# Kernel tuning notes

Hardware: AMD Instinct MI355X
Metric: run time of the kernel (lower is better)

The kernel has to match this reference:

```python
import jax, jax.numpy as jnp
import numpy as np

B, C, H, W = 16, 384, 28, 28
F, E, FFN, NB, NH, WS = 384, 384, 1536, 12, 8, 7


def setup_inputs() -> dict:
    key = jax.random.key(0)
    ks = jax.random.split(key, 16)
    g = lambda k, s: (0.02 * jax.random.normal(k, s)).astype(jnp.float32)
    inp = {}
    inp['x'] = jax.random.normal(ks[0], (B, C, H, W), jnp.float32)
    # ViTInput params
    inp['embed_w'] = g(ks[1], (2, E))
    inp['embed_b'] = jnp.zeros((E,), jnp.float32)
    inp['in_w'] = g(ks[2], (E + C, F))
    inp['in_b'] = jnp.zeros((F,), jnp.float32)
    # per-block (stacked over NB) params
    inp['ln1_s'] = jnp.ones((NB, F), jnp.float32)
    inp['ln1_b'] = jnp.zeros((NB, F), jnp.float32)
    inp['qkv_w'] = g(ks[3], (NB, F, 3 * F))
    inp['qkv_b'] = jnp.zeros((NB, 3 * F), jnp.float32)
    inp['proj_w'] = g(ks[4], (NB, F, F))
    inp['proj_b'] = jnp.zeros((NB, F), jnp.float32)
    inp['ln2_s'] = jnp.ones((NB, F), jnp.float32)
    inp['ln2_b'] = jnp.zeros((NB, F), jnp.float32)
    inp['ffn_w1'] = g(ks[5], (NB, F, FFN))
    inp['ffn_b1'] = jnp.zeros((NB, FFN), jnp.float32)
    inp['ffn_w2'] = g(ks[6], (NB, FFN, F))
    inp['ffn_b2'] = jnp.zeros((NB, F), jnp.float32)
    # rezero alpha: torch inits to 0 (identity blocks); use 0.1 to exercise compute
    inp['re_alpha'] = 0.1 * jnp.ones((NB,), jnp.float32)
    # output projection
    inp['out_w'] = g(ks[7], (F, C))
    inp['out_b'] = jnp.zeros((C,), jnp.float32)
    return inp


def _ln(x, s, b, eps=1e-5):
    m = jnp.mean(x, axis=-1, keepdims=True)
    v = jnp.mean(jnp.square(x - m), axis=-1, keepdims=True)
    return (x - m) * jax.lax.rsqrt(v + eps) * s + b


def reference(x, embed_w, embed_b, in_w, in_b, ln1_s, ln1_b, qkv_w, qkv_b,
              proj_w, proj_b, ln2_s, ln2_b, ffn_w1, ffn_b1, ffn_w2, ffn_b2,
              re_alpha, out_w, out_b):
    Bn, Cn, Hn, Wn = x.shape
    L = Hn * Wn
    tokens = x.reshape(Bn, Cn, L).transpose(0, 2, 1)  # [B, L, C]
    # Fourier pos embed (torch.meshgrid(x, y) 'ij' then row-major flatten)
    xg = jnp.repeat(jnp.arange(Wn, dtype=jnp.float32), Hn)  # [L]
    yg = jnp.tile(jnp.arange(Hn, dtype=jnp.float32), Wn)    # [L]
    xn = 2.0 * xg / (Wn - 1) - 1.0
    yn = 2.0 * yg / (Hn - 1) - 1.0
    z = jnp.stack([xn, yn], axis=-1)                         # [L, 2]
    emb = jnp.sin(z @ embed_w + embed_b)                     # [L, E]
    emb = jnp.broadcast_to(emb[None], (Bn, L, emb.shape[-1]))
    h = jnp.concatenate([emb, tokens], axis=-1) @ in_w + in_b  # [B, L, F]

    Dh = F // NH
    nW = L // WS
    scale = 1.0 / jnp.sqrt(jnp.float32(Dh))

    def block(h, p):
        (l1s, l1b, qw, qb, pw, pb, l2s, l2b, w1, b1, w2, b2, alpha) = p
        y = _ln(h, l1s, l1b)
        qkv = y @ qw + qb                                   # [B, L, 3F]
        q, k, v = jnp.split(qkv, 3, axis=-1)
        hd = lambda t: t.reshape(Bn, nW, WS, NH, Dh)
        q, k, v = hd(q), hd(k), hd(v)
        att = jnp.einsum('bwqhd,bwkhd->bwhqk', q, k) * scale  # [B,nW,H,7,7]
        att = jax.nn.softmax(att, axis=-1)
        o = jnp.einsum('bwhqk,bwkhd->bwqhd', att, v).reshape(Bn, L, NH * Dh)
        o = o @ pw + pb
        h = h + alpha * o
        y2 = _ln(h, l2s, l2b)
        y2 = jax.nn.gelu(y2 @ w1 + b1, approximate=False) @ w2 + b2
        h = h + alpha * y2
        return h, None

    h, _ = jax.lax.scan(block, h, (ln1_s, ln1_b, qkv_w, qkv_b, proj_w, proj_b,
                                   ln2_s, ln2_b, ffn_w1, ffn_b1, ffn_w2, ffn_b2,
                                   re_alpha))
    out = h @ out_w + out_b                                  # [B, L, C]
    return out.transpose(0, 2, 1).reshape(Bn, Cn, Hn, Wn)
```

## Files before the change

kernel.cpp:

```cpp
#include <hip/hip_runtime.h>
#include <hip/hip_bf16.h>
#include <cstdint>
#include <cstddef>

#define BB 16
#define CC 384
#define LL 784
#define FF 384
#define EE 384
#define FFNx 1536
#define NB 12
#define NHEAD 8
#define MM (BB * LL)
#define MBY 98

typedef __attribute__((ext_vector_type(8))) short short8;
typedef __attribute__((ext_vector_type(4))) float floatx4;
typedef __attribute__((ext_vector_type(4))) unsigned int uintx4;

__device__ __forceinline__ float bf2f(uint16_t u) {
    union { unsigned int i; float f; } v; v.i = ((unsigned int)u) << 16; return v.f;
}
__device__ __forceinline__ uint16_t f2bf(float f) {
    union { float f; unsigned int i; } v; v.f = f;
    unsigned int r = v.i + 0x7fffu + ((v.i >> 16) & 1u);
    return (uint16_t)(r >> 16);
}
__device__ __forceinline__ float load_in(const void* p, size_t i, bool bf) {
    return bf ? bf2f(((const uint16_t*)p)[i]) : ((const float*)p)[i];
}
#define PROBE_BF(probe) (((const uint16_t*)(probe))[0] == 0x3F80u)

__device__ __forceinline__ void gload_lds16(const uint16_t* g, uint16_t* l) {
    __builtin_amdgcn_global_load_lds(
        (const __attribute__((address_space(1))) uint32_t*)g,
        (__attribute__((address_space(3))) uint32_t*)l,
        16, 0, 0);
}

__device__ __forceinline__ float gelu_f(float v) {
    float y = 0.7978845608028654f * (v + 0.044715f * v * v * v);
    y = fmaxf(y, -40.f);
    float e = __expf(-2.f * y);
    float th = (1.f - e) * __builtin_amdgcn_rcpf(1.f + e);
    return 0.5f * v * (1.f + th);
}

__global__ __launch_bounds__(256) void transpose_any(const void* __restrict__ src,
                                                     uint16_t* __restrict__ dst,
                                                     int K, int N, size_t eoff,
                                                     size_t zs, size_t zd,
                                                     const uint16_t* __restrict__ probe) {
    const bool bf = PROBE_BF(probe);
    __shared__ uint16_t tile[32][33];
    size_t off = eoff + (size_t)blockIdx.z * zs;
    uint16_t* d = dst + (size_t)blockIdx.z * zd;
    int n0 = blockIdx.x * 32, k0 = blockIdx.y * 32;
    int tx = threadIdx.x & 31, ty = threadIdx.x >> 5;
#pragma unroll
    for (int i = 0; i < 32; i += 8)
        tile[ty + i][tx] = f2bf(load_in(src, off + (size_t)(k0 + ty + i) * N + (n0 + tx), bf));
    __syncthreads();
#pragma unroll
    for (int i = 0; i < 32; i += 8)
        d[(size_t)(n0 + ty + i) * K + (k0 + tx)] = tile[tx][ty + i];
}

__global__ __launch_bounds__(256) void prep_kernel(const void* __restrict__ x,
                                                   const void* __restrict__ ew,
                                                   const void* __restrict__ eb,
                                                   uint16_t* __restrict__ A0,
                                                   const uint16_t* __restrict__ probe) {
    const bool bf = PROBE_BF(probe);
    int idx = blockIdx.x * 256 + threadIdx.x;
    int row = idx / 768, col = idx - row * 768;
    int b = row / LL, l = row - b * LL;
    uint16_t v;
    if (col < EE) {
        float xn = 2.f * (float)(l / 28) / 27.f - 1.f;
        float yn = 2.f * (float)(l % 28) / 27.f - 1.f;
        float s = sinf(xn * load_in(ew, col, bf) + yn * load_in(ew, EE + col, bf)
                       + load_in(eb, col, bf));
        v = f2bf(s);
    } else {
        v = f2bf(load_in(x, ((size_t)b * CC + (col - EE)) * LL + l, bf));
    }
    A0[idx] = v;
}

__global__ __launch_bounds__(256) void ln_kernel(const float* __restrict__ h,
                                                 const void* __restrict__ sc,
                                                 const void* __restrict__ bi,
                                                 size_t eoff,
                                                 uint16_t* __restrict__ y,
                                                 const uint16_t* __restrict__ probe) {
    const bool bf = PROBE_BF(probe);
    int wave = threadIdx.x >> 6, lane = threadIdx.x & 63;
    int row = blockIdx.x * 4 + wave;
    const float* hr = h + (size_t)row * FF;
    float v[6]; float sum = 0.f;
#pragma unroll
    for (int i = 0; i < 6; ++i) { v[i] = hr[lane + 64 * i]; sum += v[i]; }
#pragma unroll
    for (int off = 32; off > 0; off >>= 1) sum += __shfl_xor(sum, off, 64);
    float mean = sum * (1.f / 384.f);
    float var = 0.f;
#pragma unroll
    for (int i = 0; i < 6; ++i) { float d = v[i] - mean; var += d * d; }
#pragma unroll
    for (int off = 32; off > 0; off >>= 1) var += __shfl_xor(var, off, 64);
    float inv = rsqrtf(var * (1.f / 384.f) + 1e-5f);
    uint16_t* yr = y + (size_t)row * FF;
#pragma unroll
    for (int i = 0; i < 6; ++i) {
        int c = lane + 64 * i;
        yr[c] = f2bf((v[i] - mean) * inv * load_in(sc, eoff + c, bf)
                     + load_in(bi, eoff + c, bf));
    }
}

__global__ __launch_bounds__(256) void resid_ln(float* __restrict__ h,
                                                const uint16_t* __restrict__ o,
                                                const void* __restrict__ sc,
                                                const void* __restrict__ bi,
                                                size_t eoff,
                                                const void* __restrict__ alpha_p, size_t aoff,
                                                uint16_t* __restrict__ y, int mirror,
                                                const uint16_t* __restrict__ probe) {
    const bool bf = PROBE_BF(probe);
    int wave = threadIdx.x >> 6, lane = threadIdx.x & 63;
    int row = blockIdx.x * 4 + wave;
    float alpha = load_in(alpha_p, aoff, bf);
    float* hr = h + (size_t)row * FF;
    const uint16_t* orr = o + (size_t)row * FF;
    float v[6]; float sum = 0.f;
#pragma unroll
    for (int i = 0; i < 6; ++i) {
        int c = lane + 64 * i;
        v[i] = hr[c] + alpha * bf2f(orr[c]);
        hr[c] = v[i];
        sum += v[i];
    }
    uint16_t* yr = y + (size_t)row * FF;
    if (mirror) {
#pragma unroll
        for (int i = 0; i < 6; ++i) yr[lane + 64 * i] = f2bf(v[i]);
        return;
    }
#pragma unroll
    for (int off = 32; off > 0; off >>= 1) sum += __shfl_xor(sum, off, 64);
    float mean = sum * (1.f / 384.f);
    float var = 0.f;
#pragma unroll
    for (int i = 0; i < 6; ++i) { float d = v[i] - mean; var += d * d; }
#pragma unroll
    for (int off = 32; off > 0; off >>= 1) var += __shfl_xor(var, off, 64);
    float inv = rsqrtf(var * (1.f / 384.f) + 1e-5f);
#pragma unroll
    for (int i = 0; i < 6; ++i) {
        int c = lane + 64 * i;
        yr[c] = f2bf((v[i] - mean) * inv * load_in(sc, eoff + c, bf)
                     + load_in(bi, eoff + c, bf));
    }
}

__global__ __launch_bounds__(256) void attn_kernel(const uint16_t* __restrict__ qkv,
                                                   uint16_t* __restrict__ o) {
    __shared__ float sm[4][1060];
    int wave = threadIdx.x >> 6, lane = threadIdx.x & 63;
    float* q = sm[wave];
    float* v = q + 2 * 336;
    float* S = q + 3 * 336;
    int gw = blockIdx.x * 4 + wave;
    int b = gw / (112 * NHEAD);
    int rem = gw - b * (112 * NHEAD);
    int w = rem >> 3, head = rem & 7;
    size_t base = ((size_t)(b * LL + w * 7)) * (3 * FF) + head * 48;
    for (int idx = lane; idx < 126; idx += 64) {
        int mat = idx / 42, c = idx - mat * 42;
        int i = c / 6, dc = c - i * 6;
        const uint16_t* src = qkv + base + (size_t)i * (3 * FF) + mat * FF + dc * 8;
        short8 vv = *(const short8*)src;
        const uint16_t* pv = (const uint16_t*)&vv;
        float* dst = q + mat * 336 + i * 48 + dc * 8;
        float4 lo, hi;
        lo.x = bf2f(pv[0]); lo.y = bf2f(pv[1]); lo.z = bf2f(pv[2]); lo.w = bf2f(pv[3]);
        hi.x = bf2f(pv[4]); hi.y = bf2f(pv[5]); hi.z = bf2f(pv[6]); hi.w = bf2f(pv[7]);
        *(float4*)dst = lo; *(float4*)(dst + 4) = hi;
    }
    __syncthreads();
    if (lane < 49) {
        int i = lane / 7, j = lane - i * 7;
        const float* k = q + 336;
        float acc = 0.f;
#pragma unroll
        for (int d = 0; d < 48; ++d) acc += q[i * 48 + d] * k[j * 48 + d];
        S[lane] = acc * 0.14433756729740643f;
    }
    __syncthreads();
    if (lane < 7) {
        int i = lane;
        float m = S[i * 7];
#pragma unroll
        for (int j = 1; j < 7; ++j) m = fmaxf(m, S[i * 7 + j]);
        float e[7]; float ssum = 0.f;
#pragma unroll
        for (int j = 0; j < 7; ++j) { e[j] = __expf(S[i * 7 + j] - m); ssum += e[j]; }
        float inv = 1.f / ssum;
#pragma unroll
        for (int j = 0; j < 7; ++j) S[i * 7 + j] = e[j] * inv;
    }
    __syncthreads();
    if (lane < 42) {
        int i = lane / 6, dc = lane - i * 6;
        float a8[8];
#pragma unroll
        for (int e = 0; e < 8; ++e) a8[e] = 0.f;
#pragma unroll
        for (int j = 0; j < 7; ++j) {
            float p = S[i * 7 + j];
            const float* vr = v + j * 48 + dc * 8;
#pragma unroll
            for (int e = 0; e < 8; ++e) a8[e] += p * vr[e];
        }
        short8 ov;
        uint16_t* po = (uint16_t*)&ov;
#pragma unroll
        for (int e = 0; e < 8; ++e) po[e] = f2bf(a8[e]);
        *(short8*)(o + ((size_t)(b * LL + w * 7 + i)) * FF + head * 48 + dc * 8) = ov;
    }
}

template <int MODE>
__global__ __launch_bounds__(256) void gemm_nt(const uint16_t* __restrict__ A,
                                               const uint16_t* __restrict__ Bt,
                                               const void* __restrict__ bias, size_t boff,
                                               float* __restrict__ Cf,
                                               uint16_t* __restrict__ Cb,
                                               const void* __restrict__ alpha_p, size_t aoff,
                                               int N, int K, int lda, int ldb, int nbx,
                                               const uint16_t* __restrict__ probe) {
    const int b = blockIdx.x;
    const int oct = b / (8 * nbx);
    const int t = b - oct * 8 * nbx;
    const int r = t & 7, nblk = t >> 3;
    const int mblk = oct * 8 + r;
    if (mblk >= MBY) return;
    const int m0 = mblk * 128, n0 = nblk * 128;

    const bool bf = PROBE_BF(probe);
    __shared__ __attribute__((aligned(16))) uint16_t lds_a[128 * 64];
    __shared__ __attribute__((aligned(16))) uint16_t lds_b[128 * 64];
    const int tid = threadIdx.x;
    const int wave = tid >> 6, lane = tid & 63;
    const int quad = lane >> 4, l16 = lane & 15;
    const int wm = (wave & 1) * 64, wn = (wave >> 1) * 64;

    floatx4 acc[4][4];
#pragma unroll
    for (int i = 0; i < 4; ++i)
#pragma unroll
        for (int j = 0; j < 4; ++j) acc[i][j] = (floatx4){0.f, 0.f, 0.f, 0.f};

    const int lrow = lane >> 3;
    const int lu = (lane & 7) ^ lrow;
    const uint16_t* Ag = A + (size_t)(m0 + wave * 32 + lrow) * lda + lu * 8;
    const uint16_t* Bg = Bt + (size_t)(n0 + wave * 32 + lrow) * ldb + lu * 8;
    uint16_t* la = &lds_a[(wave * 32) * 64];
    uint16_t* lb = &lds_b[(wave * 32) * 64];

    const int swz = l16 & 7;

    for (int k0 = 0; k0 < K; k0 += 64) {
        __syncthreads();
#pragma unroll
        for (int j = 0; j < 4; ++j) {
            gload_lds16(Ag + (size_t)j * 8 * lda + k0, la + j * 8 * 64);
            gload_lds16(Bg + (size_t)j * 8 * ldb + k0, lb + j * 8 * 64);
        }
        __syncthreads();
        short8 af[4][2], bfr[4][2];
#pragma unroll
        for (int mi = 0; mi < 4; ++mi)
#pragma unroll
            for (int kk = 0; kk < 2; ++kk)
                af[mi][kk] = *(const short8*)(&lds_a[(wm + mi * 16 + l16) * 64
                                                     + (((quad + 4 * kk) ^ swz) * 8)]);
#pragma unroll
        for (int ni = 0; ni < 4; ++ni)
#pragma unroll
            for (int kk = 0; kk < 2; ++kk)
                bfr[ni][kk] = *(const short8*)(&lds_b[(wn + ni * 16 + l16) * 64
                                                      + (((quad + 4 * kk) ^ swz) * 8)]);
#pragma unroll
        for (int kk = 0; kk < 2; ++kk)
#pragma unroll
            for (int mi = 0; mi < 4; ++mi)
#pragma unroll
                for (int ni = 0; ni < 4; ++ni)
                    acc[mi][ni] = __builtin_amdgcn_mfma_f32_16x16x32_bf16(
                        af[mi][kk], bfr[ni][kk], acc[mi][ni], 0, 0, 0);
    }

    float alpha = 0.f;
    if (MODE == 2) alpha = load_in(alpha_p, aoff, bf);
#pragma unroll
    for (int mi = 0; mi < 4; ++mi) {
#pragma unroll
        for (int ni = 0; ni < 4; ++ni) {
            int col = n0 + wn + ni * 16 + l16;
            float bcol = bias ? load_in(bias, boff + col, bf) : 0.f;
#pragma unroll
            for (int rr = 0; rr < 4; ++rr) {
                int row = m0 + wm + mi * 16 + quad * 4 + rr;
                float v = acc[mi][ni][rr] + bcol;
                if (MODE == 0) {
                    Cb[(size_t)row * N + col] = f2bf(v);
                } else if (MODE == 1) {
                    Cb[(size_t)row * N + col] = f2bf(gelu_f(v));
                } else if (MODE == 2) {
                    float hn = Cf[(size_t)row * N + col] + alpha * v;
                    Cf[(size_t)row * N + col] = hn;
                    if (Cb) Cb[(size_t)row * N + col] = f2bf(hn);
                } else if (MODE == 3) {
                    Cf[(size_t)row * N + col] = v;
                } else {
                    int bb = row / LL, l = row - bb * LL;
                    size_t oi = ((size_t)bb * CC + col) * LL + l;
                    if (bf) Cb[oi] = f2bf(v); else Cf[oi] = v;
                }
            }
        }
    }
}

#define GEMM_GRID(nbx) (104 * (nbx))

extern "C" void kernel_launch(void* const* d_in, const int* in_sizes, int n_in,
                              void* d_out, int out_size, void* d_ws, size_t ws_size,
                              hipStream_t stream) {
    const void* x        = d_in[0];
    const void* embed_w  = d_in[1];
    const void* embed_b  = d_in[2];
    const void* in_w     = d_in[3];
    const void* in_b     = d_in[4];
    const void* ln1_s    = d_in[5];
    const void* ln1_b    = d_in[6];
    const void* qkv_w    = d_in[7];
    const void* qkv_b    = d_in[8];
    const void* proj_w   = d_in[9];
    const void* proj_b   = d_in[10];
    const void* ln2_s    = d_in[11];
    const void* ln2_b    = d_in[12];
    const void* ffn_w1   = d_in[13];
    const void* ffn_b1   = d_in[14];
    const void* ffn_w2   = d_in[15];
    const void* ffn_b2   = d_in[16];
    const void* re_alpha = d_in[17];
    const void* out_w    = d_in[18];
    const void* out_b    = d_in[19];
    const uint16_t* probe = (const uint16_t*)ln1_s;

    const size_t eQKV = (size_t)3 * FF * FF;
    const size_t ePRJ = (size_t)FF * FF;
    const size_t eF1  = (size_t)FF * FFNx;
    const size_t eF2  = (size_t)FFNx * FF;
    const size_t ePB  = eQKV + ePRJ + eF1 + eF2;

    const size_t SZ_WT_ALL = ePB * NB * 2;
    const size_t SZ_WT_IN  = (size_t)768 * FF * 2;
    const size_t SZ_WT_OUT = (size_t)FF * CC * 2;
    const size_t SZ_H      = (size_t)MM * FF * 4;
    const size_t SZ_B1     = (size_t)MM * FF * 2;
    const size_t SZ_MID    = (size_t)MM * FFNx * 2;
    const size_t SZ_QKVB   = (size_t)MM * 3 * FF * 2;
    const size_t SZ_WTBLK  = ePB * 2;

    const size_t NEED_BIG   = SZ_WT_ALL + SZ_WT_IN + SZ_WT_OUT + SZ_H + SZ_B1 + SZ_MID;
    const size_t NEED_MED   = SZ_WTBLK + SZ_H + SZ_B1 + SZ_MID;
    const size_t NEED_SMALL = SZ_WTBLK + SZ_H + SZ_B1 + SZ_QKVB;
    if (ws_size < NEED_SMALL) return;

    const int layout = (ws_size >= NEED_BIG) ? 2 : (ws_size >= NEED_MED ? 1 : 0);

    char* p = (char*)d_ws;
    auto carve = [&](size_t bytes) { char* r = p; p += (bytes + 255) & ~(size_t)255; return r; };

    if (layout >= 1) {
        uint16_t *wt_qkv, *wt_proj, *wt_f1, *wt_f2, *wt_in, *wt_out;
        size_t sQ, sP, s1, s2;
        if (layout == 2) {
            uint16_t* wt_all = (uint16_t*)carve(SZ_WT_ALL);
            wt_in  = (uint16_t*)carve(SZ_WT_IN);
            wt_out = (uint16_t*)carve(SZ_WT_OUT);
            wt_qkv  = wt_all;
            wt_proj = wt_all + eQKV * NB;
            wt_f1   = wt_all + (eQKV + ePRJ) * NB;
            wt_f2   = wt_all + (eQKV + ePRJ + eF1) * NB;
            sQ = eQKV; sP = ePRJ; s1 = eF1; s2 = eF2;
        } else {
            uint16_t* wtblk = (uint16_t*)carve(SZ_WTBLK);
            wt_qkv  = wtblk;
            wt_proj = wtblk + eQKV;
            wt_f1   = wtblk + eQKV + ePRJ;
            wt_f2   = wtblk + eQKV + ePRJ + eF1;
            wt_in   = wtblk;
            wt_out  = wtblk;
            sQ = sP = s1 = s2 = 0;
        }
        float*    hbuf = (float*)carve(SZ_H);
        uint16_t* buf1 = (uint16_t*)carve(SZ_B1);
        uint16_t* bufm = (uint16_t*)carve(SZ_MID);

        if (layout == 2) {
            transpose_any<<<dim3(36, 12, NB), 256, 0, stream>>>(qkv_w, wt_qkv, FF, 3 * FF,
                                                                0, eQKV, eQKV, probe);
            transpose_any<<<dim3(12, 12, NB), 256, 0, stream>>>(proj_w, wt_proj, FF, FF,
                                                                0, ePRJ, ePRJ, probe);
            transpose_any<<<dim3(48, 12, NB), 256, 0, stream>>>(ffn_w1, wt_f1, FF, FFNx,
                                                                0, eF1, eF1, probe);
            transpose_any<<<dim3(12, 48, NB), 256, 0, stream>>>(ffn_w2, wt_f2, FFNx, FF,
                                                                0, eF2, eF2, probe);
            transpose_any<<<dim3(12, 24, 1), 256, 0, stream>>>(in_w, wt_in, 768, FF, 0, 0, 0, probe);
            transpose_any<<<dim3(12, 12, 1), 256, 0, stream>>>(out_w, wt_out, FF, CC, 0, 0, 0, probe);
        } else {
            transpose_any<<<dim3(12, 24, 1), 256, 0, stream>>>(in_w, wt_in, 768, FF, 0, 0, 0, probe);
        }

        prep_kernel<<<(MM * 768) / 256, 256, 0, stream>>>(x, embed_w, embed_b, bufm, probe);
        gemm_nt<3><<<GEMM_GRID(3), 256, 0, stream>>>(
            bufm, wt_in, in_b, 0, hbuf, nullptr, nullptr, 0, FF, 768, 768, 768, 3, probe);
        ln_kernel<<<MM / 4, 256, 0, stream>>>(hbuf, ln1_s, ln1_b, 0, buf1, probe);

        for (int nb = 0; nb < NB; ++nb) {
            if (layout == 1) {
                transpose_any<<<dim3(36, 12, 1), 256, 0, stream>>>(
                    qkv_w, wt_qkv, FF, 3 * FF, (size_t)nb * eQKV, 0, 0, probe);
                transpose_any<<<dim3(12, 12, 1), 256, 0, stream>>>(
                    proj_w, wt_proj, FF, FF, (size_t)nb * ePRJ, 0, 0, probe);
                transpose_any<<<dim3(48, 12, 1), 256, 0, stream>>>(
                    ffn_w1, wt_f1, FF, FFNx, (size_t)nb * eF1, 0, 0, probe);
                transpose_any<<<dim3(12, 48, 1), 256, 0, stream>>>(
                    ffn_w2, wt_f2, FFNx, FF, (size_t)nb * eF2, 0, 0, probe);
            }
            gemm_nt<0><<<GEMM_GRID(9), 256, 0, stream>>>(
                buf1, wt_qkv + sQ * nb, qkv_b, (size_t)nb * 3 * FF,
                nullptr, bufm, nullptr, 0, 3 * FF, FF, FF, FF, 9, probe);
            attn_kernel<<<(BB * 112 * NHEAD) / 4, 256, 0, stream>>>(bufm, buf1);
            gemm_nt<0><<<GEMM_GRID(3), 256, 0, stream>>>(
                buf1, wt_proj + sP * nb, proj_b, (size_t)nb * FF,
                nullptr, bufm, nullptr, 0, FF, FF, FF, FF, 3, probe);
            resid_ln<<<MM / 4, 256, 0, stream>>>(
                hbuf, bufm, ln2_s, ln2_b, (size_t)nb * FF, re_alpha, (size_t)nb,
                buf1, 0, probe);
            gemm_nt<1><<<GEMM_GRID(12), 256, 0, stream>>>(
                buf1, wt_f1 + s1 * nb, ffn_b1, (size_t)nb * FFNx,
                nullptr, bufm, nullptr, 0, FFNx, FF, FF, FF, 12, probe);
            gemm_nt<0><<<GEMM_GRID(3), 256, 0, stream>>>(
                bufm, wt_f2 + s2 * nb, ffn_b2, (size_t)nb * FF,
                nullptr, buf1, nullptr, 0, FF, FFNx, FFNx, FFNx, 3, probe);
            if (nb < NB - 1) {
                resid_ln<<<MM / 4, 256, 0, stream>>>(
                    hbuf, buf1, ln1_s, ln1_b, (size_t)(nb + 1) * FF, re_alpha, (size_t)nb,
                    buf1, 0, probe);
            } else {
                resid_ln<<<MM / 4, 256, 0, stream>>>(
                    hbuf, buf1, ln1_s, ln1_b, 0, re_alpha, (size_t)nb,
                    buf1, 1, probe);
            }
        }

        if (layout == 1)
            transpose_any<<<dim3(12, 12, 1), 256, 0, stream>>>(out_w, wt_out, FF, CC, 0, 0, 0, probe);
        gemm_nt<4><<<GEMM_GRID(3), 256, 0, stream>>>(
            buf1, wt_out, out_b, 0, (float*)d_out, (uint16_t*)d_out, nullptr, 0,
            CC, FF, FF, FF, 3, probe);
        return;
    }

    uint16_t* wtblk = (uint16_t*)carve(SZ_WTBLK);
    float*    hbuf  = (float*)carve(SZ_H);
    uint16_t* buf1  = (uint16_t*)carve(SZ_B1);
    uint16_t* bufm  = (uint16_t*)carve(SZ_QKVB);

    uint16_t* wt_qkv  = wtblk;
    uint16_t* wt_proj = wtblk + eQKV;
    uint16_t* wt_f1   = wtblk + eQKV + ePRJ;
    uint16_t* wt_f2   = wtblk + eQKV + ePRJ + eF1;
    uint16_t* wt_in   = wtblk;
    uint16_t* wt_out  = wtblk;

    transpose_any<<<dim3(12, 24, 1), 256, 0, stream>>>(in_w, wt_in, 768, FF, 0, 0, 0, probe);
    prep_kernel<<<(MM * 768) / 256, 256, 0, stream>>>(x, embed_w, embed_b, bufm, probe);
    gemm_nt<3><<<GEMM_GRID(3), 256, 0, stream>>>(
        bufm, wt_in, in_b, 0, hbuf, nullptr, nullptr, 0, FF, 768, 768, 768, 3, probe);

    for (int nb = 0; nb < NB; ++nb) {
        transpose_any<<<dim3(36, 12, 1), 256, 0, stream>>>(
            qkv_w, wt_qkv, FF, 3 * FF, (size_t)nb * eQKV, 0, 0, probe);
        transpose_any<<<dim3(12, 12, 1), 256, 0, stream>>>(
            proj_w, wt_proj, FF, FF, (size_t)nb * ePRJ, 0, 0, probe);
        transpose_any<<<dim3(48, 12, 1), 256, 0, stream>>>(
            ffn_w1, wt_f1, FF, FFNx, (size_t)nb * eF1, 0, 0, probe);
        transpose_any<<<dim3(12, 48, 1), 256, 0, stream>>>(
            ffn_w2, wt_f2, FFNx, FF, (size_t)nb * eF2, 0, 0, probe);

        ln_kernel<<<MM / 4, 256, 0, stream>>>(hbuf, ln1_s, ln1_b, (size_t)nb * FF, buf1, probe);
        gemm_nt<0><<<GEMM_GRID(9), 256, 0, stream>>>(
            buf1, wt_qkv, qkv_b, (size_t)nb * 3 * FF, nullptr, bufm, nullptr, 0,
            3 * FF, FF, FF, FF, 9, probe);
        attn_kernel<<<(BB * 112 * NHEAD) / 4, 256, 0, stream>>>(bufm, buf1);
        gemm_nt<2><<<GEMM_GRID(3), 256, 0, stream>>>(
            buf1, wt_proj, proj_b, (size_t)nb * FF, hbuf, nullptr, re_alpha, (size_t)nb,
            FF, FF, FF, FF, 3, probe);
        ln_kernel<<<MM / 4, 256, 0, stream>>>(hbuf, ln2_s, ln2_b, (size_t)nb * FF, buf1, probe);

        for (int ph = 0; ph < 2; ++ph) {
            gemm_nt<1><<<GEMM_GRID(6), 256, 0, stream>>>(
                buf1, wt_f1 + (size_t)ph * 768 * FF, ffn_b1,
                (size_t)nb * FFNx + (size_t)ph * 768, nullptr, bufm, nullptr, 0,
                768, FF, FF, FF, 6, probe);
            gemm_nt<2><<<GEMM_GRID(3), 256, 0, stream>>>(
                bufm, wt_f2 + (size_t)ph * 768,
                (ph == 0) ? ffn_b2 : nullptr, (size_t)nb * FF,
                hbuf, (ph == 1 && nb == NB - 1) ? buf1 : nullptr, re_alpha, (size_t)nb,
                FF, 768, 768, FFNx, 3, probe);
        }
    }

    transpose_any<<<dim3(12, 12, 1), 256, 0, stream>>>(out_w, wt_out, FF, CC, 0, 0, 0, probe);
    gemm_nt<4><<<GEMM_GRID(3), 256, 0, stream>>>(
        buf1, wt_out, out_b, 0, (float*)d_out, (uint16_t*)d_out, nullptr, 0,
        CC, FF, FF, FF, 3, probe);
}
```

Measured before the change: 2.119 ms.

## Prefetch next GEMM k-tile into registers instead of direct global-to-LDS loads

The GEMM main loop drops the direct global_load_lds transfers and stages tiles through registers. The next k-tile is loaded into registers before the current tile's MFMAs run, then written into swizzled LDS after a barrier. The aim is to hide global memory latency behind compute, since the old loop waited on each load before computing. The cost is extra VGPRs and the explicit LDS writes, which can lower occupancy.

New measurement: 2.177 ms. +2.8%, slower.

```diff
diff --git a/kernel.cpp b/kernel.cpp
--- a/kernel.cpp
+++ b/kernel.cpp
@@ -30,13 +30,6 @@
     return bf ? bf2f(((const uint16_t*)p)[i]) : ((const float*)p)[i];
 }
 #define PROBE_BF(probe) (((const uint16_t*)(probe))[0] == 0x3F80u)
-
-__device__ __forceinline__ void gload_lds16(const uint16_t* g, uint16_t* l) {
-    __builtin_amdgcn_global_load_lds(
-        (const __attribute__((address_space(1))) uint32_t*)g,
-        (__attribute__((address_space(3))) uint32_t*)l,
-        16, 0, 0);
-}
 
 __device__ __forceinline__ float gelu_f(float v) {
     float y = 0.7978845608028654f * (v + 0.044715f * v * v * v);
@@ -262,22 +255,38 @@
 #pragma unroll
         for (int j = 0; j < 4; ++j) acc[i][j] = (floatx4){0.f, 0.f, 0.f, 0.f};
 
-    const int lrow = lane >> 3;
-    const int lu = (lane & 7) ^ lrow;
-    const uint16_t* Ag = A + (size_t)(m0 + wave * 32 + lrow) * lda + lu * 8;
-    const uint16_t* Bg = Bt + (size_t)(n0 + wave * 32 + lrow) * ldb + lu * 8;
-    uint16_t* la = &lds_a[(wave * 32) * 64];
-    uint16_t* lb = &lds_b[(wave * 32) * 64];
+    const int r0 = tid >> 3;
+    const int cu = tid & 7;
+    const int ch = cu * 8;
+    const uint16_t* Ab = A + (size_t)m0 * lda;
+    const uint16_t* Bb = Bt + (size_t)n0 * ldb;
+
+    uintx4 ra[4], rb[4];
+    auto gload = [&](int k0) {
+#pragma unroll
+        for (int i = 0; i < 4; ++i) {
+            int row = r0 + i * 32;
+            ra[i] = *(const uintx4*)(Ab + (size_t)row * lda + k0 + ch);
+            rb[i] = *(const uintx4*)(Bb + (size_t)row * ldb + k0 + ch);
+        }
+    };
+    auto swrite = [&]() {
+#pragma unroll
+        for (int i = 0; i < 4; ++i) {
+            int row = r0 + i * 32;
+            int slot = (cu ^ (row & 7)) * 8;
+            *(uintx4*)(&lds_a[row * 64 + slot]) = ra[i];
+            *(uintx4*)(&lds_b[row * 64 + slot]) = rb[i];
+        }
+    };
 
     const int swz = l16 & 7;
 
+    gload(0);
+    swrite();
     for (int k0 = 0; k0 < K; k0 += 64) {
-        __syncthreads();
-#pragma unroll
-        for (int j = 0; j < 4; ++j) {
-            gload_lds16(Ag + (size_t)j * 8 * lda + k0, la + j * 8 * 64);
-            gload_lds16(Bg + (size_t)j * 8 * ldb + k0, lb + j * 8 * 64);
-        }
+        const bool more = (k0 + 64 < K);
+        if (more) gload(k0 + 64);
         __syncthreads();
         short8 af[4][2], bfr[4][2];
 #pragma unroll
@@ -300,6 +309,8 @@
                 for (int ni = 0; ni < 4; ++ni)
                     acc[mi][ni] = __builtin_amdgcn_mfma_f32_16x16x32_bf16(
                         af[mi][kk], bfr[ni][kk], acc[mi][ni], 0, 0, 0);
+        __syncthreads();
+        if (more) swrite();
     }
 
     float alpha = 0.f;
```
